# Performance work log

Measured on AMD Instinct MI355X. Metric: run time of the kernel, lower is better.

Reference implementation:

```python
import jax, jax.numpy as jnp
import numpy as np

ALPHA, GAMMA = 0.25, 2.0
CLASS_W, COORD_W, MASK_W = 2.0, 5.0, 5.0
EPS = 1e-8


def point_sample(masks, coords):
    """Bilinear sample (grid_sample, align_corners=False, zero padding).
    masks: [R, H, W]; coords: [P, 2] as (x, y) in [0, 1]. Returns [R, P]."""
    H, W = masks.shape[-2:]
    gx = 2.0 * coords[:, 0] - 1.0
    gy = 2.0 * coords[:, 1] - 1.0
    x = ((gx + 1.0) * W - 1.0) * 0.5
    y = ((gy + 1.0) * H - 1.0) * 0.5
    x0 = jnp.floor(x)
    y0 = jnp.floor(y)
    wx1 = x - x0
    wy1 = y - y0
    wx0 = 1.0 - wx1
    wy0 = 1.0 - wy1
    x0i = x0.astype(jnp.int32)
    y0i = y0.astype(jnp.int32)
    x1i = x0i + 1
    y1i = y0i + 1

    def gather(ix, iy):
        valid = ((ix >= 0) & (ix < W) & (iy >= 0) & (iy < H)).astype(masks.dtype)
        ixc = jnp.clip(ix, 0, W - 1)
        iyc = jnp.clip(iy, 0, H - 1)
        return masks[:, iyc, ixc] * valid  # [R, P]

    return (gather(x0i, y0i) * (wx0 * wy0)
            + gather(x1i, y0i) * (wx1 * wy0)
            + gather(x0i, y1i) * (wx0 * wy1)
            + gather(x1i, y1i) * (wx1 * wy1))


def setup_inputs() -> dict:
    key = jax.random.key(0)
    k1, k2, k3, k4, k5, k6 = jax.random.split(key, 6)
    bs, Q, n_ctrl, Hm, Wm, T, P = 8, 300, 16, 128, 128, 160, 12544
    return {
        "pred_logits": jax.random.normal(k1, (bs, Q, 1), jnp.float32),
        "pred_ctrl_points": jax.random.uniform(k2, (bs, Q, n_ctrl, 2), jnp.float32),
        "pred_seg_mask": jax.random.normal(k3, (bs, Q, Hm, Wm), jnp.float32),
        "tgt_pts": jax.random.uniform(k4, (T, n_ctrl, 2), jnp.float32),
        "tgt_masks": jax.random.uniform(k5, (T, Hm, Wm), jnp.float32),
        "point_coords": jax.random.uniform(k6, (P, 2), jnp.float32),
        "lvl": 0,
    }


def reference(pred_logits, pred_ctrl_points, pred_seg_mask, tgt_pts, tgt_masks, point_coords, lvl):
    bs, Q = pred_logits.shape[:2]
    out_prob = jax.nn.sigmoid(pred_logits.reshape(bs * Q, -1))          # [N, 1]
    out_pts = pred_ctrl_points.reshape(bs * Q, -1)                      # [N, 2*n_ctrl]
    tgt_flat = tgt_pts.reshape(tgt_pts.shape[0], -1)                    # [T, 2*n_ctrl]

    cost_mask_dice = 0.0
    if lvl < 2:  # num_seg_layers
        out_masks = pred_seg_mask.reshape(bs * Q, *pred_seg_mask.shape[-2:])
        # nearest-interp of tgt_masks to out_masks size is identity (same size)
        t_pts_samp = point_sample(tgt_masks, point_coords)              # [T, P]
        o_pts_samp = point_sample(out_masks, point_coords)              # [N, P]
        s = jax.nn.sigmoid(o_pts_samp)                                  # dice_loss sigmoids inputs
        numerator = 2.0 * jnp.einsum('np,tp->nt', s, t_pts_samp)        # [N, T]
        denominator = s.sum(-1)[:, None] + t_pts_samp.sum(-1)[None, :]
        cost_mask_dice = 1.0 - (numerator + 1.0) / (denominator + 1.0)

    neg_cost = (1.0 - ALPHA) * out_prob ** GAMMA * (-jnp.log(1.0 - out_prob + EPS))
    pos_cost = ALPHA * (1.0 - out_prob) ** GAMMA * (-jnp.log(out_prob + EPS))
    cost_class = pos_cost - neg_cost                                    # [N, 1]

    cost_kpts = jnp.abs(out_pts[:, None, :] - tgt_flat[None, :, :]).sum(-1)  # L1 cdist [N, T]

    C = CLASS_W * cost_class + COORD_W * cost_kpts + MASK_W * cost_mask_dice
    return C.reshape(bs, Q, -1)
```

## Files before the change

### kernel.cpp

```cpp
#include <hip/hip_runtime.h>
#include <hip/hip_bf16.h>
#include <cstdint>

#define HW 128
#define MASK_ELEMS (HW * HW)
#define SBLK 1024
#define NBLK 256

typedef unsigned short ushort_t;
typedef __attribute__((ext_vector_type(4))) unsigned short ushort4_t;
typedef __attribute__((ext_vector_type(8))) short short8;
typedef __attribute__((ext_vector_type(4))) float f32x4;

__device__ __forceinline__ float asf(unsigned int u) {
    union { unsigned int i; float f; } c;
    c.i = u;
    return c.f;
}
__device__ __forceinline__ ushort_t f2bf(float f) {
    union { float f; unsigned int i; } c;
    c.f = f;
    unsigned int r = c.i + 0x7FFFu + ((c.i >> 16) & 1u);
    return (ushort_t)(r >> 16);
}

__global__ void kprep(const float* __restrict__ coords, int* __restrict__ idx,
                      uint2* __restrict__ wpk, int P) {
    int i = blockIdx.x * 256 + threadIdx.x;
    if (i >= P) return;
    float cx = coords[2 * i], cy = coords[2 * i + 1];
    float x = cx * (float)HW - 0.5f;
    float y = cy * (float)HW - 0.5f;
    float x0f = floorf(x), y0f = floorf(y);
    float wx1 = x - x0f, wy1 = y - y0f;
    float wx0 = 1.f - wx1, wy0 = 1.f - wy1;
    int x0 = (int)x0f, y0 = (int)y0f;

    float wxA = (x0 >= 0) ? wx0 : wx1;
    float wxB = (x0 >= 0 && x0 < HW - 1) ? wx1 : 0.f;
    float wyA = (y0 >= 0) ? wy0 : wy1;
    float wyB = (y0 >= 0 && y0 < HW - 1) ? wy1 : 0.f;
    int bx = max(x0, 0), by = max(y0, 0);
    if (bx > HW - 2) { bx = HW - 2; wxB = wxA; wxA = 0.f; }
    if (by > HW - 2) { by = HW - 2; wyB = wyA; wyA = 0.f; }

    idx[i] = by * HW + bx;
    wpk[i] = make_uint2((unsigned)f2bf(wxA * wyA) | ((unsigned)f2bf(wxB * wyA) << 16),
                        (unsigned)f2bf(wxA * wyB) | ((unsigned)f2bf(wxB * wyB) << 16));
}

__device__ __forceinline__ void stage_mask(const float* __restrict__ g, float* l, int tid) {
    #pragma unroll
    for (int j = 0; j < MASK_ELEMS / (SBLK * 4); ++j) {
        int o = j * SBLK * 4 + tid * 4;
        __builtin_amdgcn_global_load_lds(
            (const __attribute__((address_space(1))) unsigned int*)(const void*)(g + o),
            (__attribute__((address_space(3))) unsigned int*)(void*)(l + o), 16, 0, 0);
    }
}

__global__ __launch_bounds__(SBLK, 4) void ksamp_all(
        const float* __restrict__ pmask, const float* __restrict__ tmasks,
        const int* __restrict__ idx, const uint2* __restrict__ wpk,
        ushort_t* __restrict__ S, ushort_t* __restrict__ tsamp,
        float* __restrict__ ssum, float* __restrict__ tsum,
        const int* __restrict__ lvl, int N, int T, int P) {
    if (*lvl >= 2) return;
    __shared__ float buf[2][MASK_ELEMS];
    __shared__ float wred[2][SBLK / 64];
    int tid = threadIdx.x;
    int NM = N + T;
    int nq = P >> 2;

    int4 idr[4];
    uint4 war[4], wbr[4];
    #pragma unroll
    for (int it = 0; it < 4; ++it) {
        int q = it * SBLK + tid;
        if (q < nq) {
            idr[it] = ((const int4*)idx)[q];
            war[it] = ((const uint4*)wpk)[2 * q];
            wbr[it] = ((const uint4*)wpk)[2 * q + 1];
        } else {
            idr[it] = make_int4(0, 0, 0, 0);
            war[it] = make_uint4(0, 0, 0, 0);
            wbr[it] = make_uint4(0, 0, 0, 0);
        }
    }

    int b = blockIdx.x;
    if (b < NM) {
        const float* m0 = (b < N) ? pmask + (size_t)b * MASK_ELEMS
                                  : tmasks + (size_t)(b - N) * MASK_ELEMS;
        stage_mask(m0, buf[0], tid);
    }
    asm volatile("s_waitcnt vmcnt(0)" ::: "memory");
    __syncthreads();

    int cur = 0, cnt = 0;
    for (int mi = b; mi < NM; mi += NBLK, ++cnt) {
        int nxt = mi + NBLK;
        if (nxt < NM) {
            const float* mn = (nxt < N) ? pmask + (size_t)nxt * MASK_ELEMS
                                        : tmasks + (size_t)(nxt - N) * MASK_ELEMS;
            stage_mask(mn, buf[cur ^ 1], tid);
        }
        const float* lm = buf[cur];
        bool sig = (mi < N);
        ushort4_t* o4 = sig ? (ushort4_t*)(S + (size_t)mi * P)
                            : (ushort4_t*)(tsamp + (size_t)(mi - N) * P);
        float sum = 0.f;
        #pragma unroll
        for (int it = 0; it < 4; ++it) {
            int q = it * SBLK + tid;
            if (q < nq) {
                float v[4];
                int bi[4] = {idr[it].x, idr[it].y, idr[it].z, idr[it].w};
                unsigned wa[4] = {war[it].x, war[it].z, wbr[it].x, wbr[it].z};
                unsigned wb[4] = {war[it].y, war[it].w, wbr[it].y, wbr[it].w};
                #pragma unroll
                for (int p2 = 0; p2 < 4; ++p2) {
                    int bb = bi[p2];
                    float t00 = lm[bb], t01 = lm[bb + 1];
                    float t10 = lm[bb + HW], t11 = lm[bb + HW + 1];
                    float vv = asf(wa[p2] << 16) * t00 + asf(wa[p2] & 0xffff0000u) * t01
                             + asf(wb[p2] << 16) * t10 + asf(wb[p2] & 0xffff0000u) * t11;
                    if (sig) vv = __builtin_amdgcn_rcpf(1.f + __expf(-vv));
                    v[p2] = vv;
                }
                ushort4_t o = {f2bf(v[0]), f2bf(v[1]), f2bf(v[2]), f2bf(v[3])};
                o4[q] = o;
                sum += (v[0] + v[1]) + (v[2] + v[3]);
            }
        }
        #pragma unroll
        for (int m2 = 32; m2 > 0; m2 >>= 1) sum += __shfl_xor(sum, m2, 64);
        if ((tid & 63) == 0) wred[cnt & 1][tid >> 6] = sum;
        asm volatile("s_waitcnt vmcnt(0)" ::: "memory");
        __syncthreads();
        if (tid == 0) {
            float s = 0.f;
            #pragma unroll
            for (int w2 = 0; w2 < SBLK / 64; ++w2) s += wred[cnt & 1][w2];
            if (sig) ssum[mi] = s;
            else tsum[mi - N] = s;
        }
        cur ^= 1;
    }
}

#define LDF(Aarr, Barr, kof)                                                              \
    do {                                                                                  \
        _Pragma("unroll") for (int m_ = 0; m_ < 3; ++m_)                                  \
            Aarr[m_] = *(const short8*)(pa + (size_t)m_ * 16 * P + (kof));                \
        _Pragma("unroll") for (int j_ = 0; j_ < 5; ++j_)                                  \
            Barr[j_] = *(const short8*)(pb + (size_t)j_ * 16 * P + (kof));                \
    } while (0)

#define FMAS(Aarr, Barr)                                                                  \
    do {                                                                                  \
        _Pragma("unroll") for (int m_ = 0; m_ < 3; ++m_) {                                \
            _Pragma("unroll") for (int j_ = 0; j_ < 5; ++j_)                              \
                acc[m_][j_] = __builtin_amdgcn_mfma_f32_16x16x32_bf16(                    \
                    Aarr[m_], Barr[j_], acc[m_][j_], 0, 0, 0);                            \
        }                                                                                 \
    } while (0)

__global__ __launch_bounds__(256) void kgemm(const ushort_t* __restrict__ S,
                                             const ushort_t* __restrict__ Tm,
                                             float* __restrict__ Cpart,
                                             const int* __restrict__ lvl,
                                             int N, int T, int P, int nsteps) {
    if (*lvl >= 2) return;
    int tid = threadIdx.x;
    int wid = tid >> 6, lane = tid & 63;
    int wm = wid >> 1, wt = wid & 1;
    int r = lane & 15, g = lane >> 4;
    int n0 = blockIdx.x * 96 + wm * 48;
    int t0 = wt * 80;
    size_t k0 = (size_t)blockIdx.y * nsteps * 32 + g * 8;
    const ushort_t* pa = S + (size_t)(n0 + r) * P + k0;
    const ushort_t* pb = Tm + (size_t)(t0 + r) * P + k0;

    f32x4 acc[3][5];
    #pragma unroll
    for (int m2 = 0; m2 < 3; ++m2)
        #pragma unroll
        for (int j2 = 0; j2 < 5; ++j2) acc[m2][j2] = (f32x4){0.f, 0.f, 0.f, 0.f};

    short8 a0[3], b0[5], a1[3], b1[5];
    LDF(a0, b0, 0);
    int ks = 0;
    for (; ks + 2 < nsteps; ks += 2) {
        LDF(a1, b1, (ks + 1) * 32);
        FMAS(a0, b0);
        LDF(a0, b0, (ks + 2) * 32);
        FMAS(a1, b1);
    }
    LDF(a1, b1, (ks + 1) * 32);
    FMAS(a0, b0);
    FMAS(a1, b1);

    size_t cb = (size_t)blockIdx.y * N * T;
    #pragma unroll
    for (int m2 = 0; m2 < 3; ++m2)
        #pragma unroll
        for (int j2 = 0; j2 < 5; ++j2)
            #pragma unroll
            for (int q = 0; q < 4; ++q) {
                int row = n0 + m2 * 16 + g * 4 + q;
                int col = t0 + j2 * 16 + r;
                Cpart[cb + (size_t)row * T + col] = acc[m2][j2][q];
            }
}

__global__ void kfinal(const float* __restrict__ logits, const float* __restrict__ opts,
                       const float* __restrict__ tpts, const float* __restrict__ Cpart,
                       const float* __restrict__ ssum, const float* __restrict__ tsum,
                       const int* __restrict__ lvl, float* __restrict__ out,
                       int N, int T, int nks) {
    int idx = blockIdx.x * 256 + threadIdx.x;
    if (idx >= N * T) return;
    int n = idx / T, t = idx - n * T;

    float lg = logits[n];
    float p = 1.f / (1.f + __expf(-lg));
    float pos = 0.25f * (1.f - p) * (1.f - p) * (-logf(p + 1e-8f));
    float neg = 0.75f * p * p * (-logf(1.f - p + 1e-8f));
    float ccls = pos - neg;

    float kp = 0.f;
    const float4* a4 = (const float4*)(opts + (size_t)n * 32);
    const float4* b4 = (const float4*)(tpts + (size_t)t * 32);
    #pragma unroll
    for (int j = 0; j < 8; ++j) {
        float4 a = a4[j], b = b4[j];
        kp += fabsf(a.x - b.x) + fabsf(a.y - b.y) + fabsf(a.z - b.z) + fabsf(a.w - b.w);
    }

    float dice = 0.f;
    if (*lvl < 2) {
        float dot = 0.f;
        for (int ks = 0; ks < nks; ++ks) dot += Cpart[(size_t)ks * N * T + idx];
        dice = 1.f - (2.f * dot + 1.f) / (ssum[n] + tsum[t] + 1.f);
    }
    out[idx] = 2.f * ccls + 5.f * kp + 5.f * dice;
}

extern "C" void kernel_launch(void* const* d_in, const int* in_sizes, int n_in,
                              void* d_out, int out_size, void* d_ws, size_t ws_size,
                              hipStream_t stream) {
    const float* logits = (const float*)d_in[0];
    const float* cpts   = (const float*)d_in[1];
    const float* pmask  = (const float*)d_in[2];
    const float* tpts   = (const float*)d_in[3];
    const float* tmasks = (const float*)d_in[4];
    const float* coords = (const float*)d_in[5];
    const int*   lvl    = (const int*)d_in[6];
    float* out = (float*)d_out;

    int N = in_sizes[0];
    int T = in_sizes[3] / 32;
    int P = in_sizes[5] / 2;

    char* w = (char*)d_ws;
    auto alloc = [&](size_t bytes) {
        char* r = w;
        w += (bytes + 255) & ~(size_t)255;
        return r;
    };
    int*      idxb  = (int*)alloc((size_t)P * 4);
    uint2*    wpkb  = (uint2*)alloc((size_t)P * 8);
    ushort_t* tsamp = (ushort_t*)alloc((size_t)T * P * 2);
    ushort_t* S     = (ushort_t*)alloc((size_t)N * P * 2);
    float*    ssumb = (float*)alloc((size_t)N * 4);
    float*    tsumb = (float*)alloc((size_t)T * 4);
    size_t base_bytes = (size_t)(w - (char*)d_ws);

    int nks = 28;
    if (base_bytes + (size_t)nks * N * T * 4 > ws_size) nks = 14;
    if (base_bytes + (size_t)nks * N * T * 4 > ws_size) nks = 7;
    int nsteps = (P / 32) / nks;
    float* Cpart = (float*)alloc((size_t)nks * N * T * 4);

    kprep<<<(P + 255) / 256, 256, 0, stream>>>(coords, idxb, wpkb, P);
    ksamp_all<<<NBLK, SBLK, 0, stream>>>(pmask, tmasks, idxb, wpkb, S, tsamp,
                                         ssumb, tsumb, lvl, N, T, P);
    kgemm<<<dim3(N / 96, nks), 256, 0, stream>>>(S, tsamp, Cpart, lvl, N, T, P, nsteps);
    kfinal<<<(N * T + 255) / 256, 256, 0, stream>>>(logits, cpts, tpts, Cpart, ssumb, tsumb,
                                                    lvl, out, N, T, nks);
}
```

Before: 120.1 us.

## Use atomic work queue for mask sampling and defer row-sum reduction

Replaces the static round-robin assignment of masks to sampling blocks with a global atomic counter, reset in the prep kernel, so blocks pull the next mask dynamically and load stays balanced across the 2560 masks. The per-block cross-wave reduction and its extra barrier are removed. Per-wave partial sums are written to a workspace array and summed in the final kernel instead. This adds an atomic per mask and 16 extra loads per output element in the final kernel.

```diff
diff --git a/kernel.cpp b/kernel.cpp
--- a/kernel.cpp
+++ b/kernel.cpp
@@ -25,7 +25,8 @@
 }
 
 __global__ void kprep(const float* __restrict__ coords, int* __restrict__ idx,
-                      uint2* __restrict__ wpk, int P) {
+                      uint2* __restrict__ wpk, int* __restrict__ ctr, int P) {
+    if (blockIdx.x == 0 && threadIdx.x == 0) *ctr = 0;
     int i = blockIdx.x * 256 + threadIdx.x;
     if (i >= P) return;
     float cx = coords[2 * i], cy = coords[2 * i + 1];
@@ -63,11 +64,11 @@
         const float* __restrict__ pmask, const float* __restrict__ tmasks,
         const int* __restrict__ idx, const uint2* __restrict__ wpk,
         ushort_t* __restrict__ S, ushort_t* __restrict__ tsamp,
-        float* __restrict__ ssum, float* __restrict__ tsum,
+        float* __restrict__ spart, int* __restrict__ ctr,
         const int* __restrict__ lvl, int N, int T, int P) {
     if (*lvl >= 2) return;
     __shared__ float buf[2][MASK_ELEMS];
-    __shared__ float wred[2][SBLK / 64];
+    __shared__ int sh_mi[2];
     int tid = threadIdx.x;
     int NM = N + T;
     int nq = P >> 2;
@@ -88,23 +89,28 @@
         }
     }
 
-    int b = blockIdx.x;
-    if (b < NM) {
-        const float* m0 = (b < N) ? pmask + (size_t)b * MASK_ELEMS
-                                  : tmasks + (size_t)(b - N) * MASK_ELEMS;
+    if (tid == 0) sh_mi[0] = atomicAdd(ctr, 1);
+    __syncthreads();
+    int mi = sh_mi[0];
+    if (mi < NM) {
+        const float* m0 = (mi < N) ? pmask + (size_t)mi * MASK_ELEMS
+                                   : tmasks + (size_t)(mi - N) * MASK_ELEMS;
         stage_mask(m0, buf[0], tid);
     }
-    asm volatile("s_waitcnt vmcnt(0)" ::: "memory");
-    __syncthreads();
-
-    int cur = 0, cnt = 0;
-    for (int mi = b; mi < NM; mi += NBLK, ++cnt) {
-        int nxt = mi + NBLK;
-        if (nxt < NM) {
-            const float* mn = (nxt < N) ? pmask + (size_t)nxt * MASK_ELEMS
-                                        : tmasks + (size_t)(nxt - N) * MASK_ELEMS;
+    if (tid == 0) sh_mi[1] = (mi < NM) ? atomicAdd(ctr, 1) : NM;
+
+    int cur = 0, p = 1;
+    while (mi < NM) {
+        asm volatile("s_waitcnt vmcnt(0)" ::: "memory");
+        __syncthreads();
+        int nmi = sh_mi[p];
+        if (nmi < NM) {
+            const float* mn = (nmi < N) ? pmask + (size_t)nmi * MASK_ELEMS
+                                        : tmasks + (size_t)(nmi - N) * MASK_ELEMS;
             stage_mask(mn, buf[cur ^ 1], tid);
         }
+        if (tid == 0) sh_mi[p ^ 1] = (nmi < NM) ? atomicAdd(ctr, 1) : NM;
+
         const float* lm = buf[cur];
         bool sig = (mi < N);
         ushort4_t* o4 = sig ? (ushort4_t*)(S + (size_t)mi * P)
@@ -135,17 +141,11 @@
         }
         #pragma unroll
         for (int m2 = 32; m2 > 0; m2 >>= 1) sum += __shfl_xor(sum, m2, 64);
-        if ((tid & 63) == 0) wred[cnt & 1][tid >> 6] = sum;
-        asm volatile("s_waitcnt vmcnt(0)" ::: "memory");
-        __syncthreads();
-        if (tid == 0) {
-            float s = 0.f;
-            #pragma unroll
-            for (int w2 = 0; w2 < SBLK / 64; ++w2) s += wred[cnt & 1][w2];
-            if (sig) ssum[mi] = s;
-            else tsum[mi - N] = s;
-        }
+        if ((tid & 63) == 0) spart[(size_t)(tid >> 6) * NM + mi] = sum;
+
+        mi = nmi;
         cur ^= 1;
+        p ^= 1;
     }
 }
 
@@ -216,7 +216,7 @@
 
 __global__ void kfinal(const float* __restrict__ logits, const float* __restrict__ opts,
                        const float* __restrict__ tpts, const float* __restrict__ Cpart,
-                       const float* __restrict__ ssum, const float* __restrict__ tsum,
+                       const float* __restrict__ spart,
                        const int* __restrict__ lvl, float* __restrict__ out,
                        int N, int T, int nks) {
     int idx = blockIdx.x * 256 + threadIdx.x;
@@ -242,7 +242,14 @@
     if (*lvl < 2) {
         float dot = 0.f;
         for (int ks = 0; ks < nks; ++ks) dot += Cpart[(size_t)ks * N * T + idx];
-        dice = 1.f - (2.f * dot + 1.f) / (ssum[n] + tsum[t] + 1.f);
+        int NM = N + T;
+        float sn = 0.f, st = 0.f;
+        #pragma unroll
+        for (int w2 = 0; w2 < SBLK / 64; ++w2) {
+            sn += spart[(size_t)w2 * NM + n];
+            st += spart[(size_t)w2 * NM + N + t];
+        }
+        dice = 1.f - (2.f * dot + 1.f) / (sn + st + 1.f);
     }
     out[idx] = 2.f * ccls + 5.f * kp + 5.f * dice;
 }
@@ -262,6 +269,7 @@
     int N = in_sizes[0];
     int T = in_sizes[3] / 32;
     int P = in_sizes[5] / 2;
+    int NM = N + T;
 
     char* w = (char*)d_ws;
     auto alloc = [&](size_t bytes) {
@@ -273,8 +281,8 @@
     uint2*    wpkb  = (uint2*)alloc((size_t)P * 8);
     ushort_t* tsamp = (ushort_t*)alloc((size_t)T * P * 2);
     ushort_t* S     = (ushort_t*)alloc((size_t)N * P * 2);
-    float*    ssumb = (float*)alloc((size_t)N * 4);
-    float*    tsumb = (float*)alloc((size_t)T * 4);
+    float*    spart = (float*)alloc((size_t)(SBLK / 64) * NM * 4);
+    int*      ctr   = (int*)alloc(256);
     size_t base_bytes = (size_t)(w - (char*)d_ws);
 
     int nks = 28;
@@ -283,10 +291,10 @@
     int nsteps = (P / 32) / nks;
     float* Cpart = (float*)alloc((size_t)nks * N * T * 4);
 
-    kprep<<<(P + 255) / 256, 256, 0, stream>>>(coords, idxb, wpkb, P);
+    kprep<<<(P + 255) / 256, 256, 0, stream>>>(coords, idxb, wpkb, ctr, P);
     ksamp_all<<<NBLK, SBLK, 0, stream>>>(pmask, tmasks, idxb, wpkb, S, tsamp,
-                                         ssumb, tsumb, lvl, N, T, P);
+                                         spart, ctr, lvl, N, T, P);
     kgemm<<<dim3(N / 96, nks), 256, 0, stream>>>(S, tsamp, Cpart, lvl, N, T, P, nsteps);
-    kfinal<<<(N * T + 255) / 256, 256, 0, stream>>>(logits, cpts, tpts, Cpart, ssumb, tsumb,
+    kfinal<<<(N * T + 255) / 256, 256, 0, stream>>>(logits, cpts, tpts, Cpart, spart,
                                                     lvl, out, N, T, nks);
 }
```

Result: slower. 131.8 us (+9.7%).

## Stage masks through registers with deeper prefetch instead of global_load_lds

Applied to the files above, without the earlier changes.

The sampling kernel stops using direct global-to-LDS loads. Masks are now loaded into two register sets up to three masks ahead, written to the LDS double buffer, and the per-mask wait on all vector memory (vmcnt) is replaced by an LDS-only wait plus a barrier. This lets global loads overlap several sampling rounds, at the cost of more registers per thread, and the min-blocks launch bound is dropped. The GEMM's K-split count also falls from 28 to 14, which halves the partial-sum traffic but leaves fewer blocks in the GEMM.

```diff
diff --git a/kernel.cpp b/kernel.cpp
--- a/kernel.cpp
+++ b/kernel.cpp
@@ -23,6 +23,12 @@
     unsigned int r = c.i + 0x7FFFu + ((c.i >> 16) & 1u);
     return (ushort_t)(r >> 16);
 }
+
+#define LDS_BARRIER()                                         \
+    do {                                                      \
+        asm volatile("s_waitcnt lgkmcnt(0)" ::: "memory");    \
+        __builtin_amdgcn_s_barrier();                         \
+    } while (0)
 
 __global__ void kprep(const float* __restrict__ coords, int* __restrict__ idx,
                       uint2* __restrict__ wpk, int P) {
@@ -49,17 +55,7 @@
                         (unsigned)f2bf(wxA * wyB) | ((unsigned)f2bf(wxB * wyB) << 16));
 }
 
-__device__ __forceinline__ void stage_mask(const float* __restrict__ g, float* l, int tid) {
-    #pragma unroll
-    for (int j = 0; j < MASK_ELEMS / (SBLK * 4); ++j) {
-        int o = j * SBLK * 4 + tid * 4;
-        __builtin_amdgcn_global_load_lds(
-            (const __attribute__((address_space(1))) unsigned int*)(const void*)(g + o),
-            (__attribute__((address_space(3))) unsigned int*)(void*)(l + o), 16, 0, 0);
-    }
-}
-
-__global__ __launch_bounds__(SBLK, 4) void ksamp_all(
+__global__ __launch_bounds__(SBLK) void ksamp_all(
         const float* __restrict__ pmask, const float* __restrict__ tmasks,
         const int* __restrict__ idx, const uint2* __restrict__ wpk,
         ushort_t* __restrict__ S, ushort_t* __restrict__ tsamp,
@@ -68,9 +64,9 @@
     if (*lvl >= 2) return;
     __shared__ float buf[2][MASK_ELEMS];
     __shared__ float wred[2][SBLK / 64];
-    int tid = threadIdx.x;
-    int NM = N + T;
-    int nq = P >> 2;
+    const int tid = threadIdx.x;
+    const int NM = N + T;
+    const int nq = P >> 2;
 
     int4 idr[4];
     uint4 war[4], wbr[4];
@@ -88,65 +84,101 @@
         }
     }
 
-    int b = blockIdx.x;
-    if (b < NM) {
-        const float* m0 = (b < N) ? pmask + (size_t)b * MASK_ELEMS
-                                  : tmasks + (size_t)(b - N) * MASK_ELEMS;
-        stage_mask(m0, buf[0], tid);
-    }
-    asm volatile("s_waitcnt vmcnt(0)" ::: "memory");
-    __syncthreads();
-
-    int cur = 0, cnt = 0;
-    for (int mi = b; mi < NM; mi += NBLK, ++cnt) {
-        int nxt = mi + NBLK;
-        if (nxt < NM) {
-            const float* mn = (nxt < N) ? pmask + (size_t)nxt * MASK_ELEMS
-                                        : tmasks + (size_t)(nxt - N) * MASK_ELEMS;
-            stage_mask(mn, buf[cur ^ 1], tid);
+    auto mptr = [&](int mi) -> const float* {
+        return (mi < N) ? pmask + (size_t)mi * MASK_ELEMS
+                        : tmasks + (size_t)(mi - N) * MASK_ELEMS;
+    };
+
+    const int b = blockIdx.x;
+    const int rounds = (NM - b + NBLK - 1) / NBLK;
+    if (rounds <= 0) return;
+
+    float4 rA[4], rB[4];
+    {
+        const float* g = mptr(b);
+        #pragma unroll
+        for (int j = 0; j < 4; ++j) rB[j] = *(const float4*)(g + j * (SBLK * 4) + tid * 4);
+        #pragma unroll
+        for (int j = 0; j < 4; ++j) *(float4*)&buf[0][j * (SBLK * 4) + tid * 4] = rB[j];
+        if (1 < rounds) {
+            const float* g1 = mptr(b + NBLK);
+            #pragma unroll
+            for (int j = 0; j < 4; ++j) rA[j] = *(const float4*)(g1 + j * (SBLK * 4) + tid * 4);
         }
-        const float* lm = buf[cur];
-        bool sig = (mi < N);
-        ushort4_t* o4 = sig ? (ushort4_t*)(S + (size_t)mi * P)
-                            : (ushort4_t*)(tsamp + (size_t)(mi - N) * P);
-        float sum = 0.f;
-        #pragma unroll
-        for (int it = 0; it < 4; ++it) {
-            int q = it * SBLK + tid;
-            if (q < nq) {
-                float v[4];
-                int bi[4] = {idr[it].x, idr[it].y, idr[it].z, idr[it].w};
-                unsigned wa[4] = {war[it].x, war[it].z, wbr[it].x, wbr[it].z};
-                unsigned wb[4] = {war[it].y, war[it].w, wbr[it].y, wbr[it].w};
-                #pragma unroll
-                for (int p2 = 0; p2 < 4; ++p2) {
-                    int bb = bi[p2];
-                    float t00 = lm[bb], t01 = lm[bb + 1];
-                    float t10 = lm[bb + HW], t11 = lm[bb + HW + 1];
-                    float vv = asf(wa[p2] << 16) * t00 + asf(wa[p2] & 0xffff0000u) * t01
-                             + asf(wb[p2] << 16) * t10 + asf(wb[p2] & 0xffff0000u) * t11;
-                    if (sig) vv = __builtin_amdgcn_rcpf(1.f + __expf(-vv));
-                    v[p2] = vv;
-                }
-                ushort4_t o = {f2bf(v[0]), f2bf(v[1]), f2bf(v[2]), f2bf(v[3])};
-                o4[q] = o;
-                sum += (v[0] + v[1]) + (v[2] + v[3]);
-            }
+        if (2 < rounds) {
+            const float* g2 = mptr(b + 2 * NBLK);
+            #pragma unroll
+            for (int j = 0; j < 4; ++j) rB[j] = *(const float4*)(g2 + j * (SBLK * 4) + tid * 4);
         }
-        #pragma unroll
-        for (int m2 = 32; m2 > 0; m2 >>= 1) sum += __shfl_xor(sum, m2, 64);
-        if ((tid & 63) == 0) wred[cnt & 1][tid >> 6] = sum;
-        asm volatile("s_waitcnt vmcnt(0)" ::: "memory");
-        __syncthreads();
-        if (tid == 0) {
-            float s = 0.f;
-            #pragma unroll
-            for (int w2 = 0; w2 < SBLK / 64; ++w2) s += wred[cnt & 1][w2];
-            if (sig) ssum[mi] = s;
-            else tsum[mi - N] = s;
-        }
-        cur ^= 1;
-    }
+    }
+    LDS_BARRIER();
+
+    #define DO_MASK(kk, R)                                                                 \
+    {                                                                                      \
+        const int cur = (kk) & 1;                                                          \
+        const int mi = b + (kk) * NBLK;                                                    \
+        if ((kk) + 1 < rounds) {                                                           \
+            _Pragma("unroll")                                                              \
+            for (int j = 0; j < 4; ++j)                                                    \
+                *(float4*)&buf[cur ^ 1][j * (SBLK * 4) + tid * 4] = R[j];                  \
+            if ((kk) + 3 < rounds) {                                                       \
+                const float* gn = mptr(b + ((kk) + 3) * NBLK);                             \
+                _Pragma("unroll")                                                          \
+                for (int j = 0; j < 4; ++j)                                                \
+                    R[j] = *(const float4*)(gn + j * (SBLK * 4) + tid * 4);                \
+            }                                                                              \
+        }                                                                                  \
+        const float* lm = &buf[cur][0];                                                    \
+        const bool sig = (mi < N);                                                         \
+        ushort4_t* o4 = sig ? (ushort4_t*)(S + (size_t)mi * P)                             \
+                            : (ushort4_t*)(tsamp + (size_t)(mi - N) * P);                  \
+        float sum = 0.f;                                                                   \
+        _Pragma("unroll")                                                                  \
+        for (int it = 0; it < 4; ++it) {                                                   \
+            int q = it * SBLK + tid;                                                       \
+            if (q < nq) {                                                                  \
+                float v[4];                                                                \
+                int bi[4] = {idr[it].x, idr[it].y, idr[it].z, idr[it].w};                   \
+                unsigned wa[4] = {war[it].x, war[it].z, wbr[it].x, wbr[it].z};              \
+                unsigned wb[4] = {war[it].y, war[it].w, wbr[it].y, wbr[it].w};              \
+                _Pragma("unroll")                                                          \
+                for (int p2 = 0; p2 < 4; ++p2) {                                           \
+                    int bb = bi[p2];                                                       \
+                    float t00 = lm[bb], t01 = lm[bb + 1];                                  \
+                    float t10 = lm[bb + HW], t11 = lm[bb + HW + 1];                        \
+                    float vv = asf(wa[p2] << 16) * t00 + asf(wa[p2] & 0xffff0000u) * t01   \
+                             + asf(wb[p2] << 16) * t10 + asf(wb[p2] & 0xffff0000u) * t11;  \
+                    if (sig) vv = __builtin_amdgcn_rcpf(1.f + __expf(-vv));                \
+                    v[p2] = vv;                                                            \
+                }                                                                          \
+                ushort4_t o = {f2bf(v[0]), f2bf(v[1]), f2bf(v[2]), f2bf(v[3])};            \
+                o4[q] = o;                                                                 \
+                sum += (v[0] + v[1]) + (v[2] + v[3]);                                      \
+            }                                                                              \
+        }                                                                                  \
+        _Pragma("unroll")                                                                  \
+        for (int m2 = 32; m2 > 0; m2 >>= 1) sum += __shfl_xor(sum, m2, 64);                \
+        if ((tid & 63) == 0) wred[(kk) & 1][tid >> 6] = sum;                               \
+        LDS_BARRIER();                                                                     \
+        if (tid == 0) {                                                                    \
+            float s = 0.f;                                                                 \
+            _Pragma("unroll")                                                              \
+            for (int w2 = 0; w2 < SBLK / 64; ++w2) s += wred[(kk) & 1][w2];                \
+            if (sig) ssum[mi] = s;                                                         \
+            else tsum[mi - N] = s;                                                         \
+        }                                                                                  \
+    }
+
+    int k = 0;
+    while (true) {
+        DO_MASK(k, rA);
+        ++k;
+        if (k >= rounds) break;
+        DO_MASK(k, rB);
+        ++k;
+        if (k >= rounds) break;
+    }
+    #undef DO_MASK
 }
 
 #define LDF(Aarr, Barr, kof)                                                              \
@@ -277,8 +309,7 @@
     float*    tsumb = (float*)alloc((size_t)T * 4);
     size_t base_bytes = (size_t)(w - (char*)d_ws);
 
-    int nks = 28;
-    if (base_bytes + (size_t)nks * N * T * 4 > ws_size) nks = 14;
+    int nks = 14;
     if (base_bytes + (size_t)nks * N * T * 4 > ws_size) nks = 7;
     int nsteps = (P / 32) / nks;
     float* Cpart = (float*)alloc((size_t)nks * N * T * 4);
```

Result: slower. 178.3 us (+48.4%).

## Stage masks as packed bf16 pairs via registers and halve GEMM k-split

Applied to the files above, without the earlier changes.

The sampling kernel no longer copies masks straight from global memory into LDS. It loads them into registers, converts each element to bf16, and packs every element together with its right neighbour into a 32-bit word, so one bilinear tap pair needs one LDS read instead of two. Prefetching moves to a register double buffer, and the barrier waits only on LDS traffic rather than on global loads. The GEMM split-K count drops from 28 to 14, which shrinks the partial buffer and the final reduction but lowers GEMM parallelism; rounding the masks to bf16 also adds sampling error.

```diff
diff --git a/kernel.cpp b/kernel.cpp
--- a/kernel.cpp
+++ b/kernel.cpp
@@ -23,6 +23,12 @@
     unsigned int r = c.i + 0x7FFFu + ((c.i >> 16) & 1u);
     return (ushort_t)(r >> 16);
 }
+
+#define LDS_BARRIER()                                         \
+    do {                                                      \
+        asm volatile("s_waitcnt lgkmcnt(0)" ::: "memory");    \
+        __builtin_amdgcn_s_barrier();                         \
+    } while (0)
 
 __global__ void kprep(const float* __restrict__ coords, int* __restrict__ idx,
                       uint2* __restrict__ wpk, int P) {
@@ -49,28 +55,43 @@
                         (unsigned)f2bf(wxA * wyB) | ((unsigned)f2bf(wxB * wyB) << 16));
 }
 
-__device__ __forceinline__ void stage_mask(const float* __restrict__ g, float* l, int tid) {
-    #pragma unroll
-    for (int j = 0; j < MASK_ELEMS / (SBLK * 4); ++j) {
-        int o = j * SBLK * 4 + tid * 4;
-        __builtin_amdgcn_global_load_lds(
-            (const __attribute__((address_space(1))) unsigned int*)(const void*)(g + o),
-            (__attribute__((address_space(3))) unsigned int*)(void*)(l + o), 16, 0, 0);
-    }
-}
-
-__global__ __launch_bounds__(SBLK, 4) void ksamp_all(
+__device__ __forceinline__ void load_mask_regs(const float* __restrict__ g, int tid,
+                                               float4 rS[4], float rN[4]) {
+    #pragma unroll
+    for (int j = 0; j < 4; ++j) {
+        int o = j * (SBLK * 4) + tid * 4;
+        rS[j] = *(const float4*)(g + o);
+        rN[j] = g[min(o + 4, MASK_ELEMS - 1)];
+    }
+}
+__device__ __forceinline__ void pack_to_lds(unsigned* l, int tid, const float4 rS[4],
+                                            const float rN[4]) {
+    #pragma unroll
+    for (int j = 0; j < 4; ++j) {
+        int o = j * (SBLK * 4) + tid * 4;
+        float4 v = rS[j];
+        unsigned bx = (unsigned)f2bf(v.x), by = (unsigned)f2bf(v.y);
+        unsigned bz = (unsigned)f2bf(v.z), bw = (unsigned)f2bf(v.w);
+        unsigned bn = (unsigned)f2bf(rN[j]);
+        uint4 e = make_uint4(bx | (by << 16), by | (bz << 16),
+                             bz | (bw << 16), bw | (bn << 16));
+        *(uint4*)&l[o] = e;
+    }
+}
+
+__attribute__((amdgpu_waves_per_eu(4, 4)))
+__global__ void __launch_bounds__(SBLK) ksamp_all(
         const float* __restrict__ pmask, const float* __restrict__ tmasks,
         const int* __restrict__ idx, const uint2* __restrict__ wpk,
         ushort_t* __restrict__ S, ushort_t* __restrict__ tsamp,
         float* __restrict__ ssum, float* __restrict__ tsum,
         const int* __restrict__ lvl, int N, int T, int P) {
     if (*lvl >= 2) return;
-    __shared__ float buf[2][MASK_ELEMS];
+    __shared__ unsigned buf[2][MASK_ELEMS];
     __shared__ float wred[2][SBLK / 64];
-    int tid = threadIdx.x;
-    int NM = N + T;
-    int nq = P >> 2;
+    const int tid = threadIdx.x;
+    const int NM = N + T;
+    const int nq = P >> 2;
 
     int4 idr[4];
     uint4 war[4], wbr[4];
@@ -88,25 +109,32 @@
         }
     }
 
-    int b = blockIdx.x;
-    if (b < NM) {
-        const float* m0 = (b < N) ? pmask + (size_t)b * MASK_ELEMS
-                                  : tmasks + (size_t)(b - N) * MASK_ELEMS;
-        stage_mask(m0, buf[0], tid);
-    }
-    asm volatile("s_waitcnt vmcnt(0)" ::: "memory");
-    __syncthreads();
-
-    int cur = 0, cnt = 0;
-    for (int mi = b; mi < NM; mi += NBLK, ++cnt) {
-        int nxt = mi + NBLK;
-        if (nxt < NM) {
-            const float* mn = (nxt < N) ? pmask + (size_t)nxt * MASK_ELEMS
-                                        : tmasks + (size_t)(nxt - N) * MASK_ELEMS;
-            stage_mask(mn, buf[cur ^ 1], tid);
+    auto mptr = [&](int mi) -> const float* {
+        return (mi < N) ? pmask + (size_t)mi * MASK_ELEMS
+                        : tmasks + (size_t)(mi - N) * MASK_ELEMS;
+    };
+
+    const int b = blockIdx.x;
+    const int rounds = (NM - b + NBLK - 1) / NBLK;
+    if (rounds <= 0) return;
+
+    float4 rS[4];
+    float rN[4];
+    load_mask_regs(mptr(b), tid, rS, rN);
+    pack_to_lds(buf[0], tid, rS, rN);
+    if (rounds > 1) load_mask_regs(mptr(b + NBLK), tid, rS, rN);
+    LDS_BARRIER();
+
+    int cur = 0;
+    for (int k = 0; k < rounds; ++k) {
+        if (k + 1 < rounds) {
+            pack_to_lds(buf[cur ^ 1], tid, rS, rN);
+            if (k + 2 < rounds)
+                load_mask_regs(mptr(b + (k + 2) * NBLK), tid, rS, rN);
         }
-        const float* lm = buf[cur];
-        bool sig = (mi < N);
+        const unsigned* lm = buf[cur];
+        const int mi = b + k * NBLK;
+        const bool sig = (mi < N);
         ushort4_t* o4 = sig ? (ushort4_t*)(S + (size_t)mi * P)
                             : (ushort4_t*)(tsamp + (size_t)(mi - N) * P);
         float sum = 0.f;
@@ -121,10 +149,12 @@
                 #pragma unroll
                 for (int p2 = 0; p2 < 4; ++p2) {
                     int bb = bi[p2];
-                    float t00 = lm[bb], t01 = lm[bb + 1];
-                    float t10 = lm[bb + HW], t11 = lm[bb + HW + 1];
-                    float vv = asf(wa[p2] << 16) * t00 + asf(wa[p2] & 0xffff0000u) * t01
-                             + asf(wb[p2] << 16) * t10 + asf(wb[p2] & 0xffff0000u) * t11;
+                    unsigned r0 = lm[bb];
+                    unsigned r1 = lm[bb + HW];
+                    float vv = asf(wa[p2] << 16) * asf(r0 << 16)
+                             + asf(wa[p2] & 0xffff0000u) * asf(r0 & 0xffff0000u)
+                             + asf(wb[p2] << 16) * asf(r1 << 16)
+                             + asf(wb[p2] & 0xffff0000u) * asf(r1 & 0xffff0000u);
                     if (sig) vv = __builtin_amdgcn_rcpf(1.f + __expf(-vv));
                     v[p2] = vv;
                 }
@@ -135,13 +165,12 @@
         }
         #pragma unroll
         for (int m2 = 32; m2 > 0; m2 >>= 1) sum += __shfl_xor(sum, m2, 64);
-        if ((tid & 63) == 0) wred[cnt & 1][tid >> 6] = sum;
-        asm volatile("s_waitcnt vmcnt(0)" ::: "memory");
-        __syncthreads();
+        if ((tid & 63) == 0) wred[k & 1][tid >> 6] = sum;
+        LDS_BARRIER();
         if (tid == 0) {
             float s = 0.f;
             #pragma unroll
-            for (int w2 = 0; w2 < SBLK / 64; ++w2) s += wred[cnt & 1][w2];
+            for (int w2 = 0; w2 < SBLK / 64; ++w2) s += wred[k & 1][w2];
             if (sig) ssum[mi] = s;
             else tsum[mi - N] = s;
         }
@@ -277,8 +306,7 @@
     float*    tsumb = (float*)alloc((size_t)T * 4);
     size_t base_bytes = (size_t)(w - (char*)d_ws);
 
-    int nks = 28;
-    if (base_bytes + (size_t)nks * N * T * 4 > ws_size) nks = 14;
+    int nks = 14;
     if (base_bytes + (size_t)nks * N * T * 4 > ws_size) nks = 7;
     int nsteps = (P / 32) / nks;
     float* Cpart = (float*)alloc((size_t)nks * N * T * 4);
```

After: 119.3 us. About the same (-0.6%).
